# Performance work log

Hardware: AMD Instinct MI355X
Metric: run time of the kernel (lower is better)

Reference implementation:

```python
import jax, jax.numpy as jnp
import numpy as np

# dims
B, TQ, NQ, DQ = 2, 32, 196, 896      # batch, chunks, queries/chunk, slow-feat dim
T, H, W, CIN = 32, 8, 8, 4           # fast feature video dims
EMB = 1024                           # fast input mapping (kv) dim
HID = 512                            # cross_attn_hidden_dim
NH = 4                               # heads
HD = HID // NH                       # head dim = 128
HALF = HD // 2                       # 64 rotary freq channels
SEC = [22, 21, 21]                   # 3D rope sections (t,h,w) over the 64 freqs
FF = 2 * HID
OUT = 896
BASE = 10000.0
QGRID = 14                           # 196 = 14x14 query spatial grid
EPS = 1e-5


def _p(key, shape, scale=0.02):
    return (jax.random.normal(key, shape, dtype=jnp.float32) * scale)


def setup_inputs() -> dict:
    key = jax.random.key(0)
    ks = jax.random.split(key, 20)
    inp = {
        "x": jax.random.normal(ks[0], (B, T, H, W, CIN), dtype=jnp.float32),
        "slow_feats": jax.random.normal(ks[1], (B, TQ, NQ, DQ), dtype=jnp.float32),
        "frame_num": jnp.full((B,), T, dtype=jnp.int32),
        # query_input_mapping: 896 -> 512
        "Wq_in": _p(ks[2], (DQ, HID)), "bq_in": jnp.zeros((HID,), jnp.float32),
        # fast input_mapping (linear): 4 -> 1024
        "Wm": _p(ks[3], (CIN, EMB)), "bm": jnp.zeros((EMB,), jnp.float32),
        # cross-attn projections
        "Wq": _p(ks[4], (HID, HID)), "bq": jnp.zeros((HID,), jnp.float32),
        "Wk": _p(ks[5], (EMB, HID)), "bk": jnp.zeros((HID,), jnp.float32),
        "Wv": _p(ks[6], (EMB, HID)), "bv": jnp.zeros((HID,), jnp.float32),
        "Wo": _p(ks[7], (HID, HID)), "bo": jnp.zeros((HID,), jnp.float32),
        # decoder layer norms + FFN (dim_feedforward = 2*hidden)
        "g1": jnp.ones((HID,), jnp.float32), "be1": jnp.zeros((HID,), jnp.float32),
        "W1": _p(ks[8], (HID, FF)), "b1": jnp.zeros((FF,), jnp.float32),
        "W2": _p(ks[9], (FF, HID)), "b2": jnp.zeros((HID,), jnp.float32),
        "g2": jnp.ones((HID,), jnp.float32), "be2": jnp.zeros((HID,), jnp.float32),
        # output MLP (mlp_depth=2): 512 -> 1024 -> GELU -> 896
        "M1": _p(ks[10], (HID, 2 * HID)), "bm1": jnp.zeros((2 * HID,), jnp.float32),
        "M2": _p(ks[11], (2 * HID, OUT)), "bm2": jnp.zeros((OUT,), jnp.float32),
    }
    return inp


def _ln(x, g, b):
    m = x.mean(-1, keepdims=True)
    v = jnp.var(x, axis=-1, keepdims=True)
    return (x - m) * jax.lax.rsqrt(v + EPS) * g + b


def _rope_cos_sin(pos):
    # pos: (N,3) float (t,h,w). Qwen2-style inv_freq over head_dim=128.
    inv_freq = 1.0 / (BASE ** (jnp.arange(0, HD, 2, dtype=jnp.float32) / HD))  # (64,)
    sel = jnp.asarray([0] * SEC[0] + [1] * SEC[1] + [2] * SEC[2])              # (64,)
    freqs = pos[:, sel] * inv_freq                                             # (N,64)
    emb = jnp.concatenate([freqs, freqs], axis=-1)                             # (N,128)
    return jnp.cos(emb), jnp.sin(emb)


def _rot_half(x):
    return jnp.concatenate([-x[..., HALF:], x[..., :HALF]], axis=-1)


def _positions():
    # query tokens: (chunk t, 14x14 grid)
    qt = jnp.repeat(jnp.arange(TQ), NQ)
    qg = jnp.tile(jnp.arange(NQ), TQ)
    q_pos = jnp.stack([qt, qg // QGRID, qg % QGRID], axis=-1).astype(jnp.float32)  # (6272,3)
    # kv tokens: (frame t, HxW grid)
    kt = jnp.repeat(jnp.arange(T), H * W)
    kg = jnp.tile(jnp.arange(H * W), T)
    k_pos = jnp.stack([kt, kg // W, kg % W], axis=-1).astype(jnp.float32)          # (2048,3)
    return q_pos, k_pos


def _forward(x, slow_feats, Wq_in, bq_in, Wm, bm, Wq, bq, Wk, bk, Wv, bv,
             Wo, bo, g1, be1, W1, b1, W2, b2, g2, be2, M1, bm1, M2, bm2):
    q_pos, k_pos = _positions()
    cos_q, sin_q = _rope_cos_sin(q_pos)   # (Nq,128)
    cos_k, sin_k = _rope_cos_sin(k_pos)   # (Nk,128)
    scale = 1.0 / jnp.sqrt(jnp.float32(HD))

    def per_sample(xi, si):
        # slow feats -> queries: (32,196,896) -> (6272,512)
        q_in = (si.reshape(TQ * NQ, DQ) @ Wq_in + bq_in)
        # fast feats -> kv tokens: (T,H,W,Cin) -> (2048,1024)
        kv = (xi.reshape(T * H * W, CIN) @ Wm + bm)
        # projections -> heads
        q = (q_in @ Wq + bq).reshape(-1, NH, HD)
        k = (kv @ Wk + bk).reshape(-1, NH, HD)
        v = (kv @ Wv + bv).reshape(-1, NH, HD)
        # 3D RoPE on q and k
        q = q * cos_q[:, None, :] + _rot_half(q) * sin_q[:, None, :]
        k = k * cos_k[:, None, :] + _rot_half(k) * sin_k[:, None, :]
        # cross attention
        attn = jnp.einsum('qhd,khd->hqk', q, k) * scale
        attn = jax.nn.softmax(attn, axis=-1)
        o = jnp.einsum('hqk,khd->qhd', attn, v).reshape(-1, HID)
        o = o @ Wo + bo
        # residual + norm + FFN + norm (post-norm decoder layer)
        h = _ln(q_in + o, g1, be1)
        ff = jax.nn.gelu(h @ W1 + b1) @ W2 + b2
        h = _ln(h + ff, g2, be2)
        # output MLP: Linear -> GELU -> Linear
        y = jax.nn.gelu(h @ M1 + bm1) @ M2 + bm2
        return y  # (6272, 896)

    return jax.vmap(per_sample)(x, slow_feats)  # (B, 6272, 896)


def reference(x, slow_feats, frame_num, Wq_in, bq_in, Wm, bm, Wq, bq, Wk, bk,
              Wv, bv, Wo, bo, g1, be1, W1, b1, W2, b2, g2, be2, M1, bm1, M2, bm2):
    # frame_num is the valid-frame count per sample; here all samples are full
    # length (frame_num == T), so no KV masking is needed.
    del frame_num
    return _forward(x, slow_feats, Wq_in, bq_in, Wm, bm, Wq, bq, Wk, bk, Wv, bv,
                    Wo, bo, g1, be1, W1, b1, W2, b2, g2, be2, M1, bm1, M2, bm2)
```

## Files before the change

### kernel.cpp

```cpp
#include <hip/hip_runtime.h>
#include <cstdint>
#include <cstddef>

#define BATCH 2
#define MQ 12544
#define ROWS_Q 6272
#define MK 4096
#define ROWS_K 2048
#define HID 512
#define NH 4
#define HD 128
#define EMB 1024
#define DQ 896
#define FF 1024
#define OUTD 896

typedef __bf16 bf16;
typedef unsigned int u32;
typedef bf16 bf16x8 __attribute__((ext_vector_type(8)));
typedef bf16 bf16x4 __attribute__((ext_vector_type(4)));
typedef float f32x4 __attribute__((ext_vector_type(4)));

enum { OP_BIAS = 0, OP_GELU = 1, OP_RES = 2 };

__device__ __forceinline__ float gelu_tanh(float x) {
    float x3 = x * x * x;
    return 0.5f * x * (1.0f + tanhf(0.7978845608028654f * (x + 0.044715f * x3)));
}

__device__ __forceinline__ void gld16(const bf16* g, bf16* l) {
    __builtin_amdgcn_global_load_lds(
        (const __attribute__((address_space(1))) unsigned int*)g,
        (__attribute__((address_space(3))) unsigned int*)l, 16, 0, 0);
}

__device__ __forceinline__ u32 pack_bf16(float a, float b) {
    union { bf16 h[2]; u32 w; } u;
    u.h[0] = (bf16)a; u.h[1] = (bf16)b;
    return u.w;
}

template <int OP, bool WF32, bool WB16>
__global__ __launch_bounds__(256) void mgemm(
    const bf16* __restrict__ A, const bf16* __restrict__ Bt,
    const float* __restrict__ bias, const float* __restrict__ res,
    float* __restrict__ Cf, bf16* __restrict__ Cb, int M, int N, int K)
{
    __shared__ __align__(16) bf16 As0[128 * 32];
    __shared__ __align__(16) bf16 As1[128 * 32];
    __shared__ __align__(16) bf16 Bs0[128 * 32];
    __shared__ __align__(16) bf16 Bs1[128 * 32];
    const int tid  = threadIdx.x;
    const int m0   = blockIdx.y * 128;
    const int n0   = blockIdx.x * 128;
    const int wave = tid >> 6, lane = tid & 63;
    const int wm = (wave >> 1) * 64, wn = (wave & 1) * 64;

    f32x4 acc[4][4] = {};

    const int srow = tid >> 2;
    const int scol = (tid & 3) * 8;
    const bf16* Ag = A  + (size_t)(m0 + srow) * K + scol;
    const bf16* Bg = Bt + (size_t)(n0 + srow) * K + scol;
    bf16* Al0 = &As0[tid * 8];
    bf16* Al1 = &As1[tid * 8];
    bf16* Bl0 = &Bs0[tid * 8];
    bf16* Bl1 = &Bs1[tid * 8];
    const size_t half = (size_t)64 * K;

    const int fr = lane & 15;
    const int kq = (lane >> 4) * 8;
    const bf16* pa0 = &As0[(wm + fr) * 32 + kq];
    const bf16* pa1 = &As1[(wm + fr) * 32 + kq];
    const bf16* pb0 = &Bs0[(wn + fr) * 32 + kq];
    const bf16* pb1 = &Bs1[(wn + fr) * 32 + kq];

    for (int k0 = 0; k0 < K; k0 += 64) {
        gld16(Ag + k0,             Al0);
        gld16(Ag + k0 + half,      Al0 + 64 * 32);
        gld16(Bg + k0,             Bl0);
        gld16(Bg + k0 + half,      Bl0 + 64 * 32);
        gld16(Ag + k0 + 32,        Al1);
        gld16(Ag + k0 + 32 + half, Al1 + 64 * 32);
        gld16(Bg + k0 + 32,        Bl1);
        gld16(Bg + k0 + 32 + half, Bl1 + 64 * 32);
        __syncthreads();

        {
            bf16x8 af[4], bfr[4];
            #pragma unroll
            for (int i = 0; i < 4; ++i) af[i]  = *(const bf16x8*)(pa0 + i * 16 * 32);
            #pragma unroll
            for (int j = 0; j < 4; ++j) bfr[j] = *(const bf16x8*)(pb0 + j * 16 * 32);
            #pragma unroll
            for (int i = 0; i < 4; ++i)
                #pragma unroll
                for (int j = 0; j < 4; ++j)
                    acc[i][j] = __builtin_amdgcn_mfma_f32_16x16x32_bf16(
                        af[i], bfr[j], acc[i][j], 0, 0, 0);
        }
        {
            bf16x8 af[4], bfr[4];
            #pragma unroll
            for (int i = 0; i < 4; ++i) af[i]  = *(const bf16x8*)(pa1 + i * 16 * 32);
            #pragma unroll
            for (int j = 0; j < 4; ++j) bfr[j] = *(const bf16x8*)(pb1 + j * 16 * 32);
            #pragma unroll
            for (int i = 0; i < 4; ++i)
                #pragma unroll
                for (int j = 0; j < 4; ++j)
                    acc[i][j] = __builtin_amdgcn_mfma_f32_16x16x32_bf16(
                        af[i], bfr[j], acc[i][j], 0, 0, 0);
        }
        __syncthreads();
    }

    const int colb = n0 + wn + (lane & 15);
    const int rowb = m0 + wm + (lane >> 4) * 4;
    #pragma unroll
    for (int i = 0; i < 4; ++i) {
        #pragma unroll
        for (int j = 0; j < 4; ++j) {
            const int c = colb + j * 16;
            const float bj = bias[c];
            #pragma unroll
            for (int r = 0; r < 4; ++r) {
                const int m = rowb + i * 16 + r;
                float v = acc[i][j][r] + bj;
                if (OP == OP_GELU) v = gelu_tanh(v);
                if (OP == OP_RES)  v += res[(size_t)m * N + c];
                if (WF32) Cf[(size_t)m * N + c] = v;
                if (WB16) Cb[(size_t)m * N + c] = (bf16)v;
            }
        }
    }
}

template <int OP, bool WF32, bool WB16>
__global__ __launch_bounds__(256) void mgemm64(
    const bf16* __restrict__ A, const bf16* __restrict__ Bt,
    const float* __restrict__ bias, const float* __restrict__ res,
    float* __restrict__ Cf, bf16* __restrict__ Cb, int M, int N, int K)
{
    __shared__ __align__(16) bf16 As0[64 * 32];
    __shared__ __align__(16) bf16 As1[64 * 32];
    __shared__ __align__(16) bf16 Bs0[128 * 32];
    __shared__ __align__(16) bf16 Bs1[128 * 32];
    const int tid  = threadIdx.x;
    const int m0   = blockIdx.y * 64;
    const int n0   = blockIdx.x * 128;
    const int wave = tid >> 6, lane = tid & 63;
    const int wm = (wave >> 1) * 32, wn = (wave & 1) * 64;

    f32x4 acc[2][4] = {};

    const int srow = tid >> 2;
    const int scol = (tid & 3) * 8;
    const bf16* Ag = A  + (size_t)(m0 + srow) * K + scol;
    const bf16* Bg = Bt + (size_t)(n0 + srow) * K + scol;
    bf16* Al0 = &As0[tid * 8];
    bf16* Al1 = &As1[tid * 8];
    bf16* Bl0 = &Bs0[tid * 8];
    bf16* Bl1 = &Bs1[tid * 8];
    const size_t half = (size_t)64 * K;

    const int fr = lane & 15;
    const int kq = (lane >> 4) * 8;
    const bf16* pa0 = &As0[(wm + fr) * 32 + kq];
    const bf16* pa1 = &As1[(wm + fr) * 32 + kq];
    const bf16* pb0 = &Bs0[(wn + fr) * 32 + kq];
    const bf16* pb1 = &Bs1[(wn + fr) * 32 + kq];

    for (int k0 = 0; k0 < K; k0 += 64) {
        gld16(Ag + k0,             Al0);
        gld16(Bg + k0,             Bl0);
        gld16(Bg + k0 + half,      Bl0 + 64 * 32);
        gld16(Ag + k0 + 32,        Al1);
        gld16(Bg + k0 + 32,        Bl1);
        gld16(Bg + k0 + 32 + half, Bl1 + 64 * 32);
        __syncthreads();

        {
            bf16x8 af[2], bfr[4];
            #pragma unroll
            for (int i = 0; i < 2; ++i) af[i]  = *(const bf16x8*)(pa0 + i * 16 * 32);
            #pragma unroll
            for (int j = 0; j < 4; ++j) bfr[j] = *(const bf16x8*)(pb0 + j * 16 * 32);
            #pragma unroll
            for (int i = 0; i < 2; ++i)
                #pragma unroll
                for (int j = 0; j < 4; ++j)
                    acc[i][j] = __builtin_amdgcn_mfma_f32_16x16x32_bf16(
                        af[i], bfr[j], acc[i][j], 0, 0, 0);
        }
        {
            bf16x8 af[2], bfr[4];
            #pragma unroll
            for (int i = 0; i < 2; ++i) af[i]  = *(const bf16x8*)(pa1 + i * 16 * 32);
            #pragma unroll
            for (int j = 0; j < 4; ++j) bfr[j] = *(const bf16x8*)(pb1 + j * 16 * 32);
            #pragma unroll
            for (int i = 0; i < 2; ++i)
                #pragma unroll
                for (int j = 0; j < 4; ++j)
                    acc[i][j] = __builtin_amdgcn_mfma_f32_16x16x32_bf16(
                        af[i], bfr[j], acc[i][j], 0, 0, 0);
        }
        __syncthreads();
    }

    const int colb = n0 + wn + (lane & 15);
    const int rowb = m0 + wm + (lane >> 4) * 4;
    #pragma unroll
    for (int i = 0; i < 2; ++i) {
        #pragma unroll
        for (int j = 0; j < 4; ++j) {
            const int c = colb + j * 16;
            const float bj = bias[c];
            #pragma unroll
            for (int r = 0; r < 4; ++r) {
                const int m = rowb + i * 16 + r;
                float v = acc[i][j][r] + bj;
                if (OP == OP_GELU) v = gelu_tanh(v);
                if (OP == OP_RES)  v += res[(size_t)m * N + c];
                if (WF32) Cf[(size_t)m * N + c] = v;
                if (WB16) Cb[(size_t)m * N + c] = (bf16)v;
            }
        }
    }
}

struct TDesc { const float* src; bf16* dst; int K; int N; int tile0; };
struct TDescs { TDesc d[9]; };

__global__ __launch_bounds__(256) void transpose_all(TDescs td)
{
    __shared__ float t[32][33];
    const int blk = blockIdx.x;
    int i = 0;
    #pragma unroll
    for (int j = 1; j < 9; ++j) if (blk >= td.d[j].tile0) i = j;
    const float* src = td.d[i].src;
    bf16* dst = td.d[i].dst;
    const int K = td.d[i].K, N = td.d[i].N;
    const int local = blk - td.d[i].tile0;
    const int ntx = N >> 5;
    const int bx = local % ntx, by = local / ntx;
    const int x = threadIdx.x & 31, y = threadIdx.x >> 5;
    #pragma unroll
    for (int p = 0; p < 32; p += 8)
        t[y + p][x] = src[(size_t)(by * 32 + y + p) * N + bx * 32 + x];
    __syncthreads();
    #pragma unroll
    for (int p = 0; p < 32; p += 8)
        dst[(size_t)(bx * 32 + y + p) * K + by * 32 + x] = (bf16)t[x][y + p];
}

__global__ __launch_bounds__(256) void cvt_kernel(
    const float* __restrict__ in, bf16* __restrict__ out, int n4)
{
    int i = blockIdx.x * 256 + threadIdx.x;
    if (i >= n4) return;
    float4 v = ((const float4*)in)[i];
    out[4 * i + 0] = (bf16)v.x;
    out[4 * i + 1] = (bf16)v.y;
    out[4 * i + 2] = (bf16)v.z;
    out[4 * i + 3] = (bf16)v.w;
}

__global__ __launch_bounds__(256) void kv_kernel(
    const float* __restrict__ x, const float* __restrict__ Wm,
    const float* __restrict__ bm, bf16* __restrict__ kv)
{
    int idx = blockIdx.x * 256 + threadIdx.x;
    int r = idx >> 10, n = idx & 1023;
    float4 xv = *(const float4*)(x + (size_t)r * 4);
    float v = bm[n] + xv.x * Wm[n] + xv.y * Wm[1024 + n]
                    + xv.z * Wm[2048 + n] + xv.w * Wm[3072 + n];
    kv[idx] = (bf16)v;
}

__global__ __launch_bounds__(256) void rope_b_kernel(
    const bf16* __restrict__ in, bf16* __restrict__ out,
    int tok, int gdiv, int wdiv, int total, float sc, int istr, int icoff)
{
    int idx = blockIdx.x * 256 + threadIdx.x;
    if (idx >= total) return;
    int row = idx >> 7;
    int r2 = idx & 127;
    int h = r2 >> 5;
    int j2 = r2 & 31;
    int j = 2 * j2;
    int n = row % tok;
    int t = n / gdiv;
    int g = n % gdiv;
    int gh = g / wdiv;
    int gw = g % wdiv;
    float pa = (j < 22) ? (float)t : (j < 43) ? (float)gh : (float)gw;
    int j1 = j + 1;
    float pb = (j1 < 22) ? (float)t : (j1 < 43) ? (float)gh : (float)gw;
    float fra = pa * exp2f(-(float)j  * 0.20762050593045954f);
    float frb = pb * exp2f(-(float)j1 * 0.20762050593045954f);
    float ca = cosf(fra), sa = sinf(fra);
    float cb = cosf(frb), sb = sinf(frb);
    size_t ibase = (size_t)row * istr + icoff + (size_t)h * 128 + j;
    size_t obase = (size_t)row * 512 + (size_t)h * 128 + j;
    union { u32 w; bf16 e[2]; } ua, ub;
    ua.w = *(const u32*)(in + ibase);
    ub.w = *(const u32*)(in + ibase + 64);
    float x1a = (float)ua.e[0], x1b = (float)ua.e[1];
    float x2a = (float)ub.e[0], x2b = (float)ub.e[1];
    *(u32*)(out + obase)      = pack_bf16((x1a * ca - x2a * sa) * sc,
                                          (x1b * cb - x2b * sb) * sc);
    *(u32*)(out + obase + 64) = pack_bf16((x2a * ca + x1a * sa) * sc,
                                          (x2b * cb + x1b * sb) * sc);
}

__global__ __launch_bounds__(256) void vt_tiled(
    const bf16* __restrict__ kv16, bf16* __restrict__ vt)
{
    __shared__ bf16 t[64][72];
    const int tt = blockIdx.x * 64;
    const int d0 = blockIdx.y * 64;
    const int bh = blockIdx.z;
    const int b = bh >> 2, h = bh & 3;
    const int rr = threadIdx.x >> 4;
    const int cc = (threadIdx.x & 15) * 4;
    #pragma unroll
    for (int p = 0; p < 4; ++p) {
        int r = rr + p * 16;
        *(bf16x4*)&t[r][cc] = *(const bf16x4*)
            (kv16 + (size_t)(b * ROWS_K + tt + r) * 1024 + 512 + h * 128 + d0 + cc);
    }
    __syncthreads();
    #pragma unroll
    for (int p = 0; p < 4; ++p) {
        int r = rr + p * 16;
        bf16x4 v;
        v[0] = t[cc + 0][r]; v[1] = t[cc + 1][r];
        v[2] = t[cc + 2][r]; v[3] = t[cc + 3][r];
        *(bf16x4*)(vt + (size_t)bh * HD * ROWS_K + (size_t)(d0 + r) * ROWS_K + tt + cc) = v;
    }
}

__global__ __launch_bounds__(256) void ln_kernel(
    float* __restrict__ xb, const float* __restrict__ g,
    const float* __restrict__ be, bf16* __restrict__ out16)
{
    int wave = threadIdx.x >> 6, lane = threadIdx.x & 63;
    size_t row = (size_t)blockIdx.x * 4 + wave;
    float* xp = xb + row * 512;
    float4 a = ((const float4*)xp)[lane];
    float4 b = ((const float4*)xp)[lane + 64];
    float s  = a.x + a.y + a.z + a.w + b.x + b.y + b.z + b.w;
    float sq = a.x*a.x + a.y*a.y + a.z*a.z + a.w*a.w
             + b.x*b.x + b.y*b.y + b.z*b.z + b.w*b.w;
    #pragma unroll
    for (int off = 32; off; off >>= 1) {
        s  += __shfl_xor(s, off);
        sq += __shfl_xor(sq, off);
    }
    float mean = s * (1.0f / 512.0f);
    float var  = sq * (1.0f / 512.0f) - mean * mean;
    float rstd = rsqrtf(var + 1e-5f);
    float4 gv1 = ((const float4*)g)[lane],  gv2 = ((const float4*)g)[lane + 64];
    float4 bv1 = ((const float4*)be)[lane], bv2 = ((const float4*)be)[lane + 64];
    a.x = (a.x - mean) * rstd * gv1.x + bv1.x;
    a.y = (a.y - mean) * rstd * gv1.y + bv1.y;
    a.z = (a.z - mean) * rstd * gv1.z + bv1.z;
    a.w = (a.w - mean) * rstd * gv1.w + bv1.w;
    b.x = (b.x - mean) * rstd * gv2.x + bv2.x;
    b.y = (b.y - mean) * rstd * gv2.y + bv2.y;
    b.z = (b.z - mean) * rstd * gv2.z + bv2.z;
    b.w = (b.w - mean) * rstd * gv2.w + bv2.w;
    ((float4*)xp)[lane]      = a;
    ((float4*)xp)[lane + 64] = b;
    bf16* op = out16 + row * 512;
    *(u32*)(op + lane * 4)       = pack_bf16(a.x, a.y);
    *(u32*)(op + lane * 4 + 2)   = pack_bf16(a.z, a.w);
    *(u32*)(op + 256 + lane * 4)     = pack_bf16(b.x, b.y);
    *(u32*)(op + 256 + lane * 4 + 2) = pack_bf16(b.z, b.w);
}

__global__ __launch_bounds__(256, 2) void mattn_kernel(
    const bf16* __restrict__ qs, const bf16* __restrict__ ks,
    const bf16* __restrict__ vt, bf16* __restrict__ outb)
{
    __shared__ __align__(16) char smem[35840];
    bf16* Ksh = (bf16*)smem;
    bf16* Vsh = (bf16*)(smem + 17408);

    const int tid = threadIdx.x;
    const int wave = tid >> 6, lane = tid & 63;
    const int quad = lane >> 4, c = lane & 15;
    const int bid = blockIdx.x;
    const int bh = bid & 7;
    const int qt = bid >> 3;
    const int h  = bh & 3;
    const int b  = bh >> 2;

    const int q0 = qt * 128 + wave * 32;
    const bf16* qg = qs + (size_t)(b * ROWS_Q + q0) * HID + h * HD;
    const bf16* kg = ks + (size_t)(b * ROWS_K) * HID + h * HD;
    const bf16* vg = vt + (size_t)(b * NH + h) * HD * ROWS_K;

    bf16x8 qf[2][4];
    #pragma unroll
    for (int n = 0; n < 2; ++n)
        #pragma unroll
        for (int s = 0; s < 4; ++s)
            qf[n][s] = *(const bf16x8*)(qg + (size_t)(n * 16 + c) * HID + s * 32 + quad * 8);

    f32x4 o[8][2] = {};
    float m_i[2] = {-1e30f, -1e30f}, l_i[2] = {0.0f, 0.0f};

    const int st_t = tid >> 2;
    const int st_d = (tid & 3) * 32;
    const int sv_d = tid >> 1;
    const int sv_t = (tid & 1) * 32;

    for (int kt = 0; kt < 32; ++kt) {
        __syncthreads();
        {
            const bf16* src = kg + (size_t)(kt * 64 + st_t) * HID + st_d;
            bf16* dst = Ksh + st_t * 136 + st_d;
            #pragma unroll
            for (int i = 0; i < 4; ++i)
                *(bf16x8*)(dst + i * 8) = *(const bf16x8*)(src + i * 8);
        }
        {
            const bf16* src = vg + (size_t)sv_d * ROWS_K + kt * 64 + sv_t;
            bf16* dst = Vsh + sv_d * 72 + sv_t;
            #pragma unroll
            for (int i = 0; i < 4; ++i)
                *(bf16x8*)(dst + i * 8) = *(const bf16x8*)(src + i * 8);
        }
        __syncthreads();

        f32x4 s[4][2] = {};
        #pragma unroll
        for (int ksi = 0; ksi < 4; ++ksi) {
            bf16x8 kf[4];
            #pragma unroll
            for (int mi = 0; mi < 4; ++mi)
                kf[mi] = *(const bf16x8*)(Ksh + (mi * 16 + c) * 136 + ksi * 32 + quad * 8);
            #pragma unroll
            for (int mi = 0; mi < 4; ++mi)
                #pragma unroll
                for (int n = 0; n < 2; ++n)
                    s[mi][n] = __builtin_amdgcn_mfma_f32_16x16x32_bf16(
                        kf[mi], qf[n][ksi], s[mi][n], 0, 0, 0);
        }

        float alpha[2];
        #pragma unroll
        for (int n = 0; n < 2; ++n) {
            float mx = -1e30f;
            #pragma unroll
            for (int mi = 0; mi < 4; ++mi)
                #pragma unroll
                for (int r = 0; r < 4; ++r) mx = fmaxf(mx, s[mi][n][r]);
            mx = fmaxf(mx, __shfl_xor(mx, 16));
            mx = fmaxf(mx, __shfl_xor(mx, 32));
            float mn = fmaxf(m_i[n], mx);
            alpha[n] = __expf(m_i[n] - mn);
            m_i[n] = mn;
            float sm = 0.0f;
            #pragma unroll
            for (int mi = 0; mi < 4; ++mi)
                #pragma unroll
                for (int r = 0; r < 4; ++r) {
                    float p = __expf(s[mi][n][r] - mn);
                    s[mi][n][r] = p;
                    sm += p;
                }
            sm += __shfl_xor(sm, 16);
            sm += __shfl_xor(sm, 32);
            l_i[n] = l_i[n] * alpha[n] + sm;
            #pragma unroll
            for (int md = 0; md < 8; ++md) {
                o[md][n][0] *= alpha[n]; o[md][n][1] *= alpha[n];
                o[md][n][2] *= alpha[n]; o[md][n][3] *= alpha[n];
            }
        }

        u32 pk[4][2][2];
        #pragma unroll
        for (int mi = 0; mi < 4; ++mi)
            #pragma unroll
            for (int n = 0; n < 2; ++n) {
                pk[mi][n][0] = pack_bf16(s[mi][n][0], s[mi][n][1]);
                pk[mi][n][1] = pack_bf16(s[mi][n][2], s[mi][n][3]);
            }
        bf16x8 pf[2][2];
        #pragma unroll
        for (int kst = 0; kst < 2; ++kst)
            #pragma unroll
            for (int n = 0; n < 2; ++n) {
                union { bf16x8 v8; u32 d[4]; } u;
                #pragma unroll
                for (int dw = 0; dw < 4; ++dw) {
                    int srcl = ((quad & 1) * 2 + (dw >> 1)) * 16 + c;
                    u32 lo = (u32)__shfl((int)pk[2 * kst][n][dw & 1], srcl);
                    u32 hi = (u32)__shfl((int)pk[2 * kst + 1][n][dw & 1], srcl);
                    u.d[dw] = (quad >= 2) ? hi : lo;
                }
                pf[kst][n] = u.v8;
            }

        #pragma unroll
        for (int kst = 0; kst < 2; ++kst)
            #pragma unroll
            for (int md = 0; md < 8; ++md) {
                bf16x8 vf = *(const bf16x8*)(Vsh + (md * 16 + c) * 72 + kst * 32 + quad * 8);
                #pragma unroll
                for (int n = 0; n < 2; ++n)
                    o[md][n] = __builtin_amdgcn_mfma_f32_16x16x32_bf16(
                        vf, pf[kst][n], o[md][n], 0, 0, 0);
            }
    }

    __syncthreads();
    bf16* Osh = (bf16*)smem + wave * (32 * 136);
    float inv[2] = {1.0f / l_i[0], 1.0f / l_i[1]};
    #pragma unroll
    for (int md = 0; md < 8; ++md)
        #pragma unroll
        for (int n = 0; n < 2; ++n)
            #pragma unroll
            for (int hh = 0; hh < 2; ++hh) {
                u32 w = pack_bf16(o[md][n][2 * hh] * inv[n], o[md][n][2 * hh + 1] * inv[n]);
                int d = md * 16 + quad * 4 + 2 * hh;
                int qq = n * 16 + c;
                *(u32*)(Osh + qq * 136 + d) = w;
            }
    __syncthreads();
    bf16* og = outb + (size_t)(b * ROWS_Q + q0) * HID + h * HD;
    #pragma unroll
    for (int i = 0; i < 8; ++i) {
        int idx = i * 64 + lane;
        int qq = idx >> 4;
        int ch = idx & 15;
        bf16x8 vv = *(const bf16x8*)(Osh + qq * 136 + ch * 8);
        *(bf16x8*)(og + (size_t)qq * HID + ch * 8) = vv;
    }
}

extern "C" void kernel_launch(void* const* d_in, const int* in_sizes, int n_in,
                              void* d_out, int out_size, void* d_ws, size_t ws_size,
                              hipStream_t stream)
{
    const float* x     = (const float*)d_in[0];
    const float* slow  = (const float*)d_in[1];
    const float* Wq_in = (const float*)d_in[3];
    const float* bq_in = (const float*)d_in[4];
    const float* Wm    = (const float*)d_in[5];
    const float* bm    = (const float*)d_in[6];
    const float* Wq    = (const float*)d_in[7];
    const float* bq    = (const float*)d_in[8];
    const float* Wk    = (const float*)d_in[9];
    const float* bk    = (const float*)d_in[10];
    const float* Wv    = (const float*)d_in[11];
    const float* bv    = (const float*)d_in[12];
    const float* Wo    = (const float*)d_in[13];
    const float* bo    = (const float*)d_in[14];
    const float* g1    = (const float*)d_in[15];
    const float* be1   = (const float*)d_in[16];
    const float* W1    = (const float*)d_in[17];
    const float* b1    = (const float*)d_in[18];
    const float* W2    = (const float*)d_in[19];
    const float* b2    = (const float*)d_in[20];
    const float* g2    = (const float*)d_in[21];
    const float* be2   = (const float*)d_in[22];
    const float* M1    = (const float*)d_in[23];
    const float* bm1   = (const float*)d_in[24];
    const float* M2    = (const float*)d_in[25];
    const float* bm2   = (const float*)d_in[26];
    float* out = (float*)d_out;

    float* q_in_f = (float*)d_ws;
    float* ob     = q_in_f + (size_t)MQ * HID;
    float* bkv    = ob + (size_t)MQ * HID;
    bf16* shared_b = (bf16*)(bkv + 1024);
    bf16* q_in_b = shared_b + (size_t)MQ * FF;
    bf16* kv_b   = q_in_b + (size_t)MQ * HID;
    bf16* h_b    = kv_b + (size_t)MK * EMB;
    bf16* q16    = h_b + (size_t)MQ * HID;
    bf16* kv16   = q16 + (size_t)MQ * HID;
    bf16* qbt    = kv16 + (size_t)MK * EMB;
    bf16* kbt    = qbt + (size_t)MQ * HID;
    bf16* Vt     = kbt + (size_t)MK * HID;
    bf16* Wq_in_t = Vt + (size_t)8 * HD * ROWS_K;
    bf16* Wq_t  = Wq_in_t + 512 * 896;
    bf16* kvw_t = Wq_t + 512 * 512;
    bf16* Wo_t  = kvw_t + 1024 * 1024;
    bf16* W1_t  = Wo_t + 512 * 512;
    bf16* W2_t  = W1_t + 1024 * 512;
    bf16* M1_t  = W2_t + 512 * 1024;
    bf16* M2_t  = M1_t + 1024 * 512;
    bf16* slow_b = shared_b;
    bf16* attn_b = shared_b;
    bf16* ff1_b  = shared_b;
    bf16* m1_b   = shared_b;

    dim3 blk(256);

    TDescs td;
    int t0 = 0;
    auto set = [&](int i, const float* s, bf16* d, int K, int N) {
        td.d[i] = {s, d, K, N, t0};
        t0 += (N / 32) * (K / 32);
    };
    set(0, Wq_in, Wq_in_t, 896, 512);
    set(1, Wq,    Wq_t,    512, 512);
    set(2, Wk,    kvw_t,              1024, 512);
    set(3, Wv,    kvw_t + 512 * 1024, 1024, 512);
    set(4, Wo,    Wo_t,    512, 512);
    set(5, W1,    W1_t,    512, 1024);
    set(6, W2,    W2_t,    1024, 512);
    set(7, M1,    M1_t,    512, 1024);
    set(8, M2,    M2_t,    1024, 896);
    transpose_all<<<t0, blk, 0, stream>>>(td);

    hipMemcpyAsync(bkv,       bk, 512 * sizeof(float), hipMemcpyDeviceToDevice, stream);
    hipMemcpyAsync(bkv + 512, bv, 512 * sizeof(float), hipMemcpyDeviceToDevice, stream);

    cvt_kernel<<<(MQ * DQ / 4 + 255) / 256, blk, 0, stream>>>(slow, slow_b, MQ * DQ / 4);
    kv_kernel<<<(MK * EMB) / 256, blk, 0, stream>>>(x, Wm, bm, kv_b);

    mgemm64<OP_BIAS, true, true><<<dim3(4, 196), blk, 0, stream>>>(
        slow_b, Wq_in_t, bq_in, nullptr, q_in_f, q_in_b, MQ, HID, DQ);
    mgemm64<OP_BIAS, false, true><<<dim3(4, 196), blk, 0, stream>>>(
        q_in_b, Wq_t, bq, nullptr, nullptr, q16, MQ, HID, HID);
    mgemm64<OP_BIAS, false, true><<<dim3(8, 64), blk, 0, stream>>>(
        kv_b, kvw_t, bkv, nullptr, nullptr, kv16, MK, 1024, EMB);
    rope_b_kernel<<<(MQ * 128 + 255) / 256, blk, 0, stream>>>(
        q16, qbt, ROWS_Q, 196, 14, MQ * 128, 0.08838834764831843f, 512, 0);
    rope_b_kernel<<<(MK * 128 + 255) / 256, blk, 0, stream>>>(
        kv16, kbt, ROWS_K, 64, 8, MK * 128, 1.0f, 1024, 0);
    vt_tiled<<<dim3(32, 2, 8), blk, 0, stream>>>(kv16, Vt);
    mattn_kernel<<<dim3(392), blk, 0, stream>>>(qbt, kbt, Vt, attn_b);
    mgemm64<OP_RES, true, false><<<dim3(4, 196), blk, 0, stream>>>(
        attn_b, Wo_t, bo, q_in_f, ob, nullptr, MQ, HID, HID);
    ln_kernel<<<MQ / 4, blk, 0, stream>>>(ob, g1, be1, h_b);
    mgemm<OP_GELU, false, true><<<dim3(8, 98), blk, 0, stream>>>(
        h_b, W1_t, b1, nullptr, nullptr, ff1_b, MQ, FF, HID);
    mgemm64<OP_RES, true, false><<<dim3(4, 196), blk, 0, stream>>>(
        ff1_b, W2_t, b2, ob, q_in_f, nullptr, MQ, HID, FF);
    ln_kernel<<<MQ / 4, blk, 0, stream>>>(q_in_f, g2, be2, h_b);
    mgemm<OP_GELU, false, true><<<dim3(8, 98), blk, 0, stream>>>(
        h_b, M1_t, bm1, nullptr, nullptr, m1_b, MQ, 2 * HID, HID);
    mgemm<OP_BIAS, true, false><<<dim3(7, 98), blk, 0, stream>>>(
        m1_b, M2_t, bm2, nullptr, out, nullptr, MQ, OUTD, 2 * HID);
}
```

Measured before the change: 569.9 us.

## Software-pipeline GEMM K-loop halves and precompute rope cos/sin table

```diff
diff --git a/kernel.cpp b/kernel.cpp
--- a/kernel.cpp
+++ b/kernel.cpp
@@ -75,17 +75,17 @@
     const bf16* pb0 = &Bs0[(wn + fr) * 32 + kq];
     const bf16* pb1 = &Bs1[(wn + fr) * 32 + kq];
 
+    gld16(Ag,        Al0);
+    gld16(Ag + half, Al0 + 64 * 32);
+    gld16(Bg,        Bl0);
+    gld16(Bg + half, Bl0 + 64 * 32);
+
     for (int k0 = 0; k0 < K; k0 += 64) {
-        gld16(Ag + k0,             Al0);
-        gld16(Ag + k0 + half,      Al0 + 64 * 32);
-        gld16(Bg + k0,             Bl0);
-        gld16(Bg + k0 + half,      Bl0 + 64 * 32);
+        __syncthreads();
         gld16(Ag + k0 + 32,        Al1);
         gld16(Ag + k0 + 32 + half, Al1 + 64 * 32);
         gld16(Bg + k0 + 32,        Bl1);
         gld16(Bg + k0 + 32 + half, Bl1 + 64 * 32);
-        __syncthreads();
-
         {
             bf16x8 af[4], bfr[4];
             #pragma unroll
@@ -99,6 +99,13 @@
                     acc[i][j] = __builtin_amdgcn_mfma_f32_16x16x32_bf16(
                         af[i], bfr[j], acc[i][j], 0, 0, 0);
         }
+        __syncthreads();
+        if (k0 + 64 < K) {
+            gld16(Ag + k0 + 64,        Al0);
+            gld16(Ag + k0 + 64 + half, Al0 + 64 * 32);
+            gld16(Bg + k0 + 64,        Bl0);
+            gld16(Bg + k0 + 64 + half, Bl0 + 64 * 32);
+        }
         {
             bf16x8 af[4], bfr[4];
             #pragma unroll
@@ -112,7 +119,6 @@
                     acc[i][j] = __builtin_amdgcn_mfma_f32_16x16x32_bf16(
                         af[i], bfr[j], acc[i][j], 0, 0, 0);
         }
-        __syncthreads();
     }
 
     const int colb = n0 + wn + (lane & 15);
@@ -171,15 +177,15 @@
     const bf16* pb0 = &Bs0[(wn + fr) * 32 + kq];
     const bf16* pb1 = &Bs1[(wn + fr) * 32 + kq];
 
+    gld16(Ag,        Al0);
+    gld16(Bg,        Bl0);
+    gld16(Bg + half, Bl0 + 64 * 32);
+
     for (int k0 = 0; k0 < K; k0 += 64) {
-        gld16(Ag + k0,             Al0);
-        gld16(Bg + k0,             Bl0);
-        gld16(Bg + k0 + half,      Bl0 + 64 * 32);
+        __syncthreads();
         gld16(Ag + k0 + 32,        Al1);
         gld16(Bg + k0 + 32,        Bl1);
         gld16(Bg + k0 + 32 + half, Bl1 + 64 * 32);
-        __syncthreads();
-
         {
             bf16x8 af[2], bfr[4];
             #pragma unroll
@@ -193,6 +199,12 @@
                     acc[i][j] = __builtin_amdgcn_mfma_f32_16x16x32_bf16(
                         af[i], bfr[j], acc[i][j], 0, 0, 0);
         }
+        __syncthreads();
+        if (k0 + 64 < K) {
+            gld16(Ag + k0 + 64,        Al0);
+            gld16(Bg + k0 + 64,        Bl0);
+            gld16(Bg + k0 + 64 + half, Bl0 + 64 * 32);
+        }
         {
             bf16x8 af[2], bfr[4];
             #pragma unroll
@@ -206,7 +218,6 @@
                     acc[i][j] = __builtin_amdgcn_mfma_f32_16x16x32_bf16(
                         af[i], bfr[j], acc[i][j], 0, 0, 0);
         }
-        __syncthreads();
     }
 
     const int colb = n0 + wn + (lane & 15);
@@ -280,8 +291,18 @@
     kv[idx] = (bf16)v;
 }
 
+__global__ __launch_bounds__(256) void rope_tab_kernel(float2* __restrict__ tab)
+{
+    int i = blockIdx.x * 256 + threadIdx.x;
+    if (i >= 64 * 32) return;
+    int f = i >> 5, pos = i & 31;
+    float ang = (float)pos * exp2f(-(float)f * 0.20762050593045954f);
+    tab[i] = make_float2(cosf(ang), sinf(ang));
+}
+
 __global__ __launch_bounds__(256) void rope_b_kernel(
     const bf16* __restrict__ in, bf16* __restrict__ out,
+    const float2* __restrict__ tab,
     int tok, int gdiv, int wdiv, int total, float sc, int istr, int icoff)
 {
     int idx = blockIdx.x * 256 + threadIdx.x;
@@ -296,13 +317,13 @@
     int g = n % gdiv;
     int gh = g / wdiv;
     int gw = g % wdiv;
-    float pa = (j < 22) ? (float)t : (j < 43) ? (float)gh : (float)gw;
     int j1 = j + 1;
-    float pb = (j1 < 22) ? (float)t : (j1 < 43) ? (float)gh : (float)gw;
-    float fra = pa * exp2f(-(float)j  * 0.20762050593045954f);
-    float frb = pb * exp2f(-(float)j1 * 0.20762050593045954f);
-    float ca = cosf(fra), sa = sinf(fra);
-    float cb = cosf(frb), sb = sinf(frb);
+    int pa_i = (j < 22)  ? t : (j < 43)  ? gh : gw;
+    int pb_i = (j1 < 22) ? t : (j1 < 43) ? gh : gw;
+    float2 ta = tab[j * 32 + pa_i];
+    float2 tb = tab[j1 * 32 + pb_i];
+    float ca = ta.x, sa = ta.y;
+    float cb = tb.x, sb = tb.y;
     size_t ibase = (size_t)row * istr + icoff + (size_t)h * 128 + j;
     size_t obase = (size_t)row * 512 + (size_t)h * 128 + j;
     union { u32 w; bf16 e[2]; } ua, ub;
@@ -603,6 +624,8 @@
     bf16* ff1_b  = shared_b;
     bf16* m1_b   = shared_b;
 
+    float2* rtab = (float2*)ob;
+
     dim3 blk(256);
 
     TDescs td;
@@ -625,6 +648,7 @@
     hipMemcpyAsync(bkv,       bk, 512 * sizeof(float), hipMemcpyDeviceToDevice, stream);
     hipMemcpyAsync(bkv + 512, bv, 512 * sizeof(float), hipMemcpyDeviceToDevice, stream);
 
+    rope_tab_kernel<<<8, blk, 0, stream>>>(rtab);
     cvt_kernel<<<(MQ * DQ / 4 + 255) / 256, blk, 0, stream>>>(slow, slow_b, MQ * DQ / 4);
     kv_kernel<<<(MK * EMB) / 256, blk, 0, stream>>>(x, Wm, bm, kv_b);
 
@@ -635,9 +659,9 @@
     mgemm64<OP_BIAS, false, true><<<dim3(8, 64), blk, 0, stream>>>(
         kv_b, kvw_t, bkv, nullptr, nullptr, kv16, MK, 1024, EMB);
     rope_b_kernel<<<(MQ * 128 + 255) / 256, blk, 0, stream>>>(
-        q16, qbt, ROWS_Q, 196, 14, MQ * 128, 0.08838834764831843f, 512, 0);
+        q16, qbt, rtab, ROWS_Q, 196, 14, MQ * 128, 0.08838834764831843f, 512, 0);
     rope_b_kernel<<<(MK * 128 + 255) / 256, blk, 0, stream>>>(
-        kv16, kbt, ROWS_K, 64, 8, MK * 128, 1.0f, 1024, 0);
+        kv16, kbt, rtab, ROWS_K, 64, 8, MK * 128, 1.0f, 1024, 0);
     vt_tiled<<<dim3(32, 2, 8), blk, 0, stream>>>(kv16, Vt);
     mattn_kernel<<<dim3(392), blk, 0, stream>>>(qbt, kbt, Vt, attn_b);
     mgemm64<OP_RES, true, false><<<dim3(4, 196), blk, 0, stream>>>(
```

After: 565.8 us. No clear change (-0.7%).
